# Performance work log

Measured on AMD Instinct MI355X. Metric: run time of the kernel, lower is better.

## Reference

```python
import jax, jax.numpy as jnp
import numpy as np

INVALID = 1e9  # distance value marking a missing arc (>= 1e6 threshold in source)
TEMPERATURE = 0.5


def setup_inputs() -> dict:
    n = 4096
    key = jax.random.key(0)
    k_d, k_m, k_l = jax.random.split(key, 3)
    dist = jax.random.uniform(k_d, (n, n), dtype=jnp.float32, minval=0.0, maxval=100.0)
    keep = jax.random.uniform(k_m, (n, n)) < 0.5
    distance_matrix = jnp.where(keep, dist, INVALID).astype(jnp.float32)
    logits = (-2.0 + 0.5 * jax.random.normal(k_l, (n, n))).astype(jnp.float32)
    attention_logits = jnp.zeros((n, n), dtype=jnp.float32)
    return {
        "distance_matrix": distance_matrix,
        "logits": logits,
        "attention_logits": attention_logits,
        "source": 0,
        "destination": n - 1,
    }


def reference(distance_matrix, logits, attention_logits, source, destination):
    n = distance_matrix.shape[0]
    valid = (distance_matrix < 1e6).astype(jnp.float32)
    density = jnp.sum(valid) / (n * n)
    mu1 = 1.0
    mu2 = 10.0 * (1.0 + density)
    mu3 = 10.0 * (1.0 + density)

    # decision matrix (dense branch)
    attention = jax.nn.softmax(attention_logits, axis=1)
    x = jax.nn.sigmoid(logits / TEMPERATURE) * attention * valid  # [n, n]

    # flow penalty: vectorized form of the per-node loop
    out_flow = jnp.sum(x, axis=1)  # [n]
    in_flow = jnp.sum(x, axis=0)   # [n]
    d = out_flow - in_flow
    d = d.at[source].add(-1.0).at[destination].add(1.0)
    flow_penalty = jnp.sum(d * d)

    path_cost = jnp.sum(distance_matrix * x)  # invalid arcs have x == 0
    binary_penalty = jnp.sum(x * (1.0 - x))

    # connectivity: 10-step matmul power iteration (min(n-1, 10) = 10 for n > 11)
    reach = x
    for _ in range(10):
        reach = jnp.minimum(reach + reach @ x, 1.0)
    connectivity_penalty = jnp.square(1.0 - reach[source, destination])

    sparsity_penalty = jnp.sum(x) / (n * n)
    n_edges = jnp.sum(valid)

    return (mu1 * path_cost / (n_edges + 1e-6)
            + mu2 * flow_penalty / n
            + mu3 * binary_penalty / (n * n)
            + 20.0 * connectivity_penalty
            + 5.0 * sparsity_penalty)
```

## Files before the change

kernel.cpp:

```cpp
#include <hip/hip_runtime.h>
#include <hip/hip_bf16.h>
#include <cmath>

typedef unsigned short u16;
typedef unsigned int u32;

__device__ __forceinline__ float bf2f(u16 b) {
    return __uint_as_float(((u32)b) << 16);
}
__device__ __forceinline__ u16 f2bf(float f) {
    u32 u = __float_as_uint(f);
    u = (u + 0x7fffu + ((u >> 16) & 1u)) >> 16;
    return (u16)u;
}

__device__ __forceinline__ float wave_sum(float v) {
#pragma unroll
    for (int o = 32; o > 0; o >>= 1) v += __shfl_xor(v, o, 64);
    return v;
}

__device__ float block_sum(float v) {
    __shared__ float s[4];
    v = wave_sum(v);
    __syncthreads();
    if ((threadIdx.x & 63) == 0) s[threadIdx.x >> 6] = v;
    __syncthreads();
    return s[0] + s[1] + s[2] + s[3];
}

template <int K>
__global__ __launch_bounds__(256, 4) void k_x(
    const float* __restrict__ dist, const float* __restrict__ logit,
    const float* __restrict__ attn, const int* __restrict__ srcp,
    u16* __restrict__ xb, float* __restrict__ out_flow,
    float* __restrict__ cnt_row, float* __restrict__ s2_row,
    float* __restrict__ pc_row, float* __restrict__ v,
    float* __restrict__ izrow, int n) {
    const int row = blockIdx.x;
    const int t = threadIdx.x;
    const int lane = t & 63;
    const int wv = t >> 6;
    const size_t base = (size_t)row * n;
    const int src = *srcp;

    float4 a4[K], d4[K], l4[K];
#pragma unroll
    for (int k = 0; k < K; ++k) {
        const int col = 4 * t + 1024 * k;
        a4[k] = *(const float4*)(attn + base + col);
        d4[k] = *(const float4*)(dist + base + col);
        l4[k] = *(const float4*)(logit + base + col);
    }

    float se = 0.f, cnt = 0.f, s1 = 0.f, s2 = 0.f, pc = 0.f;
#pragma unroll
    for (int k = 0; k < K; ++k) {
        const int col = 4 * t + 1024 * k;
        const float ev[4] = {__expf(a4[k].x), __expf(a4[k].y),
                             __expf(a4[k].z), __expf(a4[k].w)};
        const float dv[4] = {d4[k].x, d4[k].y, d4[k].z, d4[k].w};
        const float lv[4] = {l4[k].x, l4[k].y, l4[k].z, l4[k].w};
        float yv[4];
        ushort4 pk;
        u16* pkp = (u16*)&pk;
#pragma unroll
        for (int q = 0; q < 4; ++q) {
            float valid = (dv[q] < 1.0e6f) ? 1.f : 0.f;
            float sg = 1.0f / (1.0f + __expf(-2.0f * lv[q]));
            float y = sg * ev[q] * valid;
            yv[q] = y;
            se += ev[q];
            cnt += valid;
            s1 += y;
            s2 += y * y;
            pc += dv[q] * y;
            pkp[q] = f2bf(y);
        }
        *(ushort4*)(xb + base + col) = pk;
        if (row == src) {
            float4 vf; vf.x = yv[0]; vf.y = yv[1]; vf.z = yv[2]; vf.w = yv[3];
            *(float4*)(v + col) = vf;
        }
    }

    se = wave_sum(se);
    cnt = wave_sum(cnt);
    s1 = wave_sum(s1);
    s2 = wave_sum(s2);
    pc = wave_sum(pc);
    __shared__ float red[4][5];
    if (lane == 0) {
        red[wv][0] = se; red[wv][1] = cnt; red[wv][2] = s1;
        red[wv][3] = s2; red[wv][4] = pc;
    }
    __syncthreads();
    if (t == 0) {
        const float SE = red[0][0] + red[1][0] + red[2][0] + red[3][0];
        const float CN = red[0][1] + red[1][1] + red[2][1] + red[3][1];
        const float S1 = red[0][2] + red[1][2] + red[2][2] + red[3][2];
        const float S2 = red[0][3] + red[1][3] + red[2][3] + red[3][3];
        const float PC = red[0][4] + red[1][4] + red[2][4] + red[3][4];
        const float iz = 1.0f / SE;
        izrow[row] = iz;
        out_flow[row] = S1 * iz;
        cnt_row[row] = CN;
        s2_row[row] = S2 * iz * iz;
        pc_row[row] = PC * iz;
    }
}

template <int FIRST>
__global__ __launch_bounds__(256) void k_iter(
    const u16* __restrict__ xb, const float* __restrict__ v_in,
    const float* __restrict__ up_in, float* __restrict__ v_out,
    float* __restrict__ up_out, float* __restrict__ ip,
    const float* __restrict__ izrow, const int* __restrict__ srcp,
    int n, int nbx, int rc) {
    __shared__ float vl[64];
    __shared__ float wz[64];
    __shared__ float vparts[4][64];
    const int t = threadIdx.x;
    const int lin = blockIdx.x;
    const int xcd = lin & 7;
    const int slot = lin >> 3;
    const int bx = slot % nbx;
    const int by = xcd * ((gridDim.x >> 3) / nbx) + slot / nbx;
    const int rows_per = n / rc;
    const int i0 = by * rows_per;
    const int j0 = bx * 1024 + t * 4;

    if (FIRST) {
        if (t < rows_per) {
            const float iz_src = izrow[*srcp];
            const float a = v_in[i0 + t] * iz_src;
            const float iz = izrow[i0 + t];
            vl[t] = a * iz;
            wz[t] = iz;
            if (bx == 0) v_out[i0 + t] = a;
        }
    } else {
        const int i = t & 63, g = t >> 6;
        const int cpg = rc >> 2;
        float a = 0.f;
#pragma unroll 4
        for (int c = g * cpg; c < (g + 1) * cpg; ++c)
            a += up_in[(size_t)c * n + i0 + i];
        vparts[g][i] = a;
        __syncthreads();
        if (t < rows_per) {
            const float s = v_in[i0 + t] + vparts[0][t] + vparts[1][t] +
                            vparts[2][t] + vparts[3][t];
            vl[t] = s * izrow[i0 + t];
            if (bx == 0) v_out[i0 + t] = s;
        }
    }
    __syncthreads();

    float4 acc = {0.f, 0.f, 0.f, 0.f};
    float4 cs = {0.f, 0.f, 0.f, 0.f};
#pragma unroll 8
    for (int i = 0; i < rows_per; ++i) {
        ushort4 xv = *(const ushort4*)(xb + (size_t)(i0 + i) * n + j0);
        float vi = vl[i];
        acc.x = fmaf(vi, bf2f(xv.x), acc.x);
        acc.y = fmaf(vi, bf2f(xv.y), acc.y);
        acc.z = fmaf(vi, bf2f(xv.z), acc.z);
        acc.w = fmaf(vi, bf2f(xv.w), acc.w);
        if (FIRST) {
            float wi = wz[i];
            cs.x = fmaf(wi, bf2f(xv.x), cs.x);
            cs.y = fmaf(wi, bf2f(xv.y), cs.y);
            cs.z = fmaf(wi, bf2f(xv.z), cs.z);
            cs.w = fmaf(wi, bf2f(xv.w), cs.w);
        }
    }
    *(float4*)(up_out + (size_t)by * n + j0) = acc;
    if (FIRST) *(float4*)(ip + (size_t)by * n + j0) = cs;
}

__global__ __launch_bounds__(256) void k_reduce(
    const float* __restrict__ out_flow, const float* __restrict__ ip,
    const float* __restrict__ cnt_row, const float* __restrict__ s2_row,
    const float* __restrict__ pc_row, const int* __restrict__ srcp,
    const int* __restrict__ dstp, float* __restrict__ pb, int n, int nchunk) {
    const int t = threadIdx.x;
    const int j = blockIdx.x * 256 + t;
    const int src = *srcp, dst = *dstp;
    float infl = 0.f;
#pragma unroll 8
    for (int c = 0; c < nchunk; ++c) infl += ip[(size_t)c * n + j];
    float d = out_flow[j] - infl;
    if (j == src) d -= 1.f;
    if (j == dst) d += 1.f;
    float f = block_sum(d * d);
    float s1 = block_sum(out_flow[j]);
    float cnt = block_sum(cnt_row[j]);
    float s2 = block_sum(s2_row[j]);
    float pc = block_sum(pc_row[j]);
    if (t == 0) {
        float* p = pb + blockIdx.x * 5;
        p[0] = f; p[1] = s1; p[2] = cnt; p[3] = s2; p[4] = pc;
    }
}

__global__ __launch_bounds__(256) void k_final(
    const float* __restrict__ pb, const float* __restrict__ v_last,
    const float* __restrict__ up_last, const int* __restrict__ dstp,
    float* __restrict__ out, int n, int nblk, int nchunk) {
    const int t = threadIdx.x;
    const int dst = *dstp;
    float flow = block_sum(t < nblk ? pb[t * 5 + 0] : 0.f);
    float S1   = block_sum(t < nblk ? pb[t * 5 + 1] : 0.f);
    float NE   = block_sum(t < nblk ? pb[t * 5 + 2] : 0.f);
    float S2   = block_sum(t < nblk ? pb[t * 5 + 3] : 0.f);
    float PC   = block_sum(t < nblk ? pb[t * 5 + 4] : 0.f);
    float r = block_sum(t < nchunk ? up_last[(size_t)t * n + dst] : 0.f);
    if (t == 0) {
        r += v_last[dst];
        float nf = (float)n;
        float nn = nf * nf;
        float density = NE / nn;
        float mu2 = 10.f * (1.f + density);
        float om = 1.f - r;
        float res = PC / (NE + 1e-6f)
                  + mu2 * flow / nf
                  + mu2 * (S1 - S2) / nn
                  + 20.f * om * om
                  + 5.f * S1 / nn;
        out[0] = res;
    }
}

extern "C" void kernel_launch(void* const* d_in, const int* in_sizes, int n_in,
                              void* d_out, int out_size, void* d_ws, size_t ws_size,
                              hipStream_t stream) {
    const float* dist = (const float*)d_in[0];
    const float* logit = (const float*)d_in[1];
    const float* attn = (const float*)d_in[2];
    const int* srcp = (const int*)d_in[3];
    const int* dstp = (const int*)d_in[4];
    const int n = (int)(std::sqrt((double)in_sizes[0]) + 0.5);
    const size_t nn = (size_t)n * n;

    const int RC = 64;
    const int nbx = n / 1024;

    char* ws = (char*)d_ws;
    u16* xb = (u16*)ws;
    float* f = (float*)(ws + nn * sizeof(u16));
    float* out_flow = f; f += n;
    float* cnt_row = f;  f += n;
    float* s2_row = f;   f += n;
    float* pc_row = f;   f += n;
    float* vA = f;       f += n;
    float* vB = f;       f += n;
    float* izrow = f;    f += n;
    float* upA = f;      f += (size_t)RC * n;
    float* upB = f;      f += (size_t)RC * n;
    float* ip = f;       f += (size_t)RC * n;
    float* pb = f;       f += 128;

    switch (n >> 10) {
        case 4: k_x<4><<<n, 256, 0, stream>>>(dist, logit, attn, srcp, xb,
                    out_flow, cnt_row, s2_row, pc_row, vA, izrow, n); break;
        case 2: k_x<2><<<n, 256, 0, stream>>>(dist, logit, attn, srcp, xb,
                    out_flow, cnt_row, s2_row, pc_row, vA, izrow, n); break;
        case 8: k_x<8><<<n, 256, 0, stream>>>(dist, logit, attn, srcp, xb,
                    out_flow, cnt_row, s2_row, pc_row, vA, izrow, n); break;
        default: k_x<1><<<n, 256, 0, stream>>>(dist, logit, attn, srcp, xb,
                    out_flow, cnt_row, s2_row, pc_row, vA, izrow, n); break;
    }

    const int niblk = nbx * RC;

    k_iter<1><<<niblk, 256, 0, stream>>>(xb, vA, nullptr, vB, upA, ip,
                                         izrow, srcp, n, nbx, RC);
    float* vin = vB;  float* uin = upA;
    float* vout;      float* uout;
    for (int it = 2; it <= 10; ++it) {
        vout = (it & 1) ? vB : vA;
        uout = (it & 1) ? upA : upB;
        k_iter<0><<<niblk, 256, 0, stream>>>(xb, vin, uin, vout, uout, nullptr,
                                             izrow, srcp, n, nbx, RC);
        vin = vout; uin = uout;
    }

    k_reduce<<<n / 256, 256, 0, stream>>>(out_flow, ip, cnt_row, s2_row,
                                          pc_row, srcp, dstp, pb, n, RC);
    k_final<<<1, 256, 0, stream>>>(pb, vin, uin, dstp, (float*)d_out, n,
                                   n / 256, RC);
}
```

Measured before the change: 125.0 us.

## Double-buffer row loads into LDS via global_load_lds in k_x

Replaces the register-held preload of all row tiles with a double-buffered pipeline that streams attention, distance and logit tiles straight into shared memory using global_load_lds, prefetching the next tile while computing the current one. The aim is to overlap memory latency with compute and cut register pressure, dropping the min-blocks launch bound. It adds LDS traffic and a block barrier per tile. Whether the loads are complete when the barrier passes depends on the compiler inserting the right vmcnt waits.

```diff
diff --git a/kernel.cpp b/kernel.cpp
--- a/kernel.cpp
+++ b/kernel.cpp
@@ -29,38 +29,58 @@
     return s[0] + s[1] + s[2] + s[3];
 }
 
-template <int K>
-__global__ __launch_bounds__(256, 4) void k_x(
+template <int NT>
+__global__ __launch_bounds__(256) void k_x(
     const float* __restrict__ dist, const float* __restrict__ logit,
     const float* __restrict__ attn, const int* __restrict__ srcp,
     u16* __restrict__ xb, float* __restrict__ out_flow,
     float* __restrict__ cnt_row, float* __restrict__ s2_row,
     float* __restrict__ pc_row, float* __restrict__ v,
     float* __restrict__ izrow, int n) {
+    __shared__ float smem[2][3][1024];
+    __shared__ float red[4][5];
     const int row = blockIdx.x;
     const int t = threadIdx.x;
     const int lane = t & 63;
     const int wv = t >> 6;
     const size_t base = (size_t)row * n;
     const int src = *srcp;
-
-    float4 a4[K], d4[K], l4[K];
+    const bool is_src = (row == src);
+
+    auto stage = [&](int tile, int buf) {
+        const int c = tile * 1024 + wv * 256 + lane * 4;
+        __builtin_amdgcn_global_load_lds(
+            (const __attribute__((address_space(1))) void*)(attn + base + c),
+            (__attribute__((address_space(3))) void*)&smem[buf][0][wv * 256],
+            16, 0, 0);
+        __builtin_amdgcn_global_load_lds(
+            (const __attribute__((address_space(1))) void*)(dist + base + c),
+            (__attribute__((address_space(3))) void*)&smem[buf][1][wv * 256],
+            16, 0, 0);
+        __builtin_amdgcn_global_load_lds(
+            (const __attribute__((address_space(1))) void*)(logit + base + c),
+            (__attribute__((address_space(3))) void*)&smem[buf][2][wv * 256],
+            16, 0, 0);
+    };
+
+    float se = 0.f, cnt = 0.f, s1 = 0.f, s2 = 0.f, pc = 0.f;
+
+    stage(0, 0);
+    __syncthreads();
+    int cur = 0;
 #pragma unroll
-    for (int k = 0; k < K; ++k) {
-        const int col = 4 * t + 1024 * k;
-        a4[k] = *(const float4*)(attn + base + col);
-        d4[k] = *(const float4*)(dist + base + col);
-        l4[k] = *(const float4*)(logit + base + col);
-    }
-
-    float se = 0.f, cnt = 0.f, s1 = 0.f, s2 = 0.f, pc = 0.f;
-#pragma unroll
-    for (int k = 0; k < K; ++k) {
-        const int col = 4 * t + 1024 * k;
-        const float ev[4] = {__expf(a4[k].x), __expf(a4[k].y),
-                             __expf(a4[k].z), __expf(a4[k].w)};
-        const float dv[4] = {d4[k].x, d4[k].y, d4[k].z, d4[k].w};
-        const float lv[4] = {l4[k].x, l4[k].y, l4[k].z, l4[k].w};
+    for (int tt = 0; tt < NT; ++tt) {
+        if (tt + 1 < NT) stage(tt + 1, cur ^ 1);
+
+        const int idx = wv * 256 + lane * 4;
+        const float4 af = *(const float4*)&smem[cur][0][idx];
+        const float4 df = *(const float4*)&smem[cur][1][idx];
+        const float4 lf = *(const float4*)&smem[cur][2][idx];
+        const int col = tt * 1024 + idx;
+        const float ev[4] = {__expf(af.x), __expf(af.y),
+                             __expf(af.z), __expf(af.w)};
+        const float dv[4] = {df.x, df.y, df.z, df.w};
+        const float lv[4] = {lf.x, lf.y, lf.z, lf.w};
         float yv[4];
         ushort4 pk;
         u16* pkp = (u16*)&pk;
@@ -78,10 +98,13 @@
             pkp[q] = f2bf(y);
         }
         *(ushort4*)(xb + base + col) = pk;
-        if (row == src) {
+        if (is_src) {
             float4 vf; vf.x = yv[0]; vf.y = yv[1]; vf.z = yv[2]; vf.w = yv[3];
             *(float4*)(v + col) = vf;
         }
+
+        __syncthreads();
+        cur ^= 1;
     }
 
     se = wave_sum(se);
@@ -89,7 +112,6 @@
     s1 = wave_sum(s1);
     s2 = wave_sum(s2);
     pc = wave_sum(pc);
-    __shared__ float red[4][5];
     if (lane == 0) {
         red[wv][0] = se; red[wv][1] = cnt; red[wv][2] = s1;
         red[wv][3] = s2; red[wv][4] = pc;
```

New measurement: 126.6 us. About the same (+1.3%).
